# Kernel tuning notes

Hardware: AMD Instinct MI355X
Metric: run time of the kernel (lower is better)

The kernel has to match this reference:

```python
import math
import jax, jax.numpy as jnp
import numpy as np

TOP_K, NC, ALPHA, BETA, EPS = 10, 80, 0.5, 6.0, 1e-9
IMG, STRIDES = 640, (8, 16, 32)


def _ciou(box1, box2, eps=1e-7):
    # box1: gt [bs,n,1,4], box2: pred [bs,1,na,4] -> [bs,n,na,1]
    b1x1, b1y1, b1x2, b1y2 = jnp.split(box1, 4, axis=-1)
    b2x1, b2y1, b2x2, b2y2 = jnp.split(box2, 4, axis=-1)
    w1, h1 = b1x2 - b1x1, b1y2 - b1y1 + eps
    w2, h2 = b2x2 - b2x1, b2y2 - b2y1 + eps
    inter = jnp.clip(jnp.minimum(b1x2, b2x2) - jnp.maximum(b1x1, b2x1), 0.0) * \
            jnp.clip(jnp.minimum(b1y2, b2y2) - jnp.maximum(b1y1, b2y1), 0.0)
    union = w1 * h1 + w2 * h2 - inter + eps
    iou = inter / union
    cw = jnp.maximum(b1x2, b2x2) - jnp.minimum(b1x1, b2x1)
    ch = jnp.maximum(b1y2, b2y2) - jnp.minimum(b1y1, b2y1)
    c2 = cw ** 2 + ch ** 2 + eps
    rho2 = ((b2x1 + b2x2 - b1x1 - b1x2) ** 2 + (b2y1 + b2y2 - b1y1 - b1y2) ** 2) / 4.0
    v = (4.0 / math.pi ** 2) * (jnp.arctan(w2 / h2) - jnp.arctan(w1 / h1)) ** 2
    alpha = jax.lax.stop_gradient(v / (v - iou + (1.0 + eps)))
    return iou - (rho2 / c2 + v * alpha)


def _assign(score, p_box, anchors, gt_labels, gt_box, mask):
    bs, na, nc = score.shape
    n = gt_box.shape[1]
    labels = gt_labels[..., 0].astype(jnp.int32)      # [bs,n]
    valid = mask > 0                                  # [bs,n,1] valid-gt mask
    # --- candidate mask: anchor center strictly inside gt box ---
    lt, rb = gt_box[..., :2], gt_box[..., 2:]
    d = jnp.concatenate([anchors[None, None] - lt[:, :, None],
                         rb[:, :, None] - anchors[None, None]], -1)  # [bs,n,na,4]
    mask_in_gts = d.min(-1) > 1e-9                    # [bs,n,na]
    mask_gts = mask_in_gts & valid
    # --- per-(gt,anchor) class score and CIoU overlap ---
    gathered = score[jnp.arange(bs)[:, None], :, labels]          # [bs,n,na]
    bbox_scores = jnp.where(mask_gts, gathered, 0.0)
    ov = _ciou(gt_box[:, :, None], p_box[:, None])[..., 0]        # [bs,n,na]
    overlaps = jnp.where(mask_gts, jnp.clip(ov, 0.0), 0.0)
    metric = jnp.where(mask_gts,
                       jnp.where(mask_gts, gathered, 1.0) ** ALPHA * overlaps ** BETA,
                       0.0)
    # --- top-k candidates per gt; suppress duplicated indices ---
    _, top_id = jax.lax.top_k(metric, TOP_K)          # [bs,n,TOP_K]
    top_id = jnp.where(valid, top_id, 0)
    bi = jnp.arange(bs)[:, None, None]
    ni = jnp.arange(n)[None, :, None]
    count = jnp.zeros((bs, n, na), jnp.int32).at[bi, ni, top_id].add(1)
    count = jnp.where(count > 1, 0, count)
    mask_pos = count.astype(metric.dtype) * mask_in_gts.astype(metric.dtype) * mask  # [bs,n,na]
    fg = mask_pos.sum(1)                              # [bs,na]
    # --- resolve anchors claimed by multiple gts via max overlap ---
    max_over = (jnp.arange(n)[None, :, None] == jnp.argmax(overlaps, 1)[:, None, :]).astype(metric.dtype)
    mask_pos = jnp.where(fg[:, None, :] > 1, max_over, mask_pos)
    fg = mask_pos.sum(1)
    # --- gather targets ---
    gt_idx = jnp.argmax(mask_pos, 1)                  # [bs,na]
    target_labels = jnp.clip(jnp.take_along_axis(labels, gt_idx, 1), 0)
    target_bboxes = jnp.take_along_axis(gt_box, gt_idx[..., None], 1)  # [bs,na,4]
    ts = jax.nn.one_hot(target_labels, NC, dtype=metric.dtype)
    ts = jnp.where(fg[..., None] > 0, ts, 0.0)
    # --- task-aligned score normalization ---
    metric = metric * mask_pos
    pos_metrics = metric.max(-1, keepdims=True)
    pos_overlaps = (overlaps * mask_pos).max(-1, keepdims=True)
    norm_metric = metric * pos_overlaps / (pos_metrics + EPS)
    target_scores = ts * norm_metric.max(1)[..., None]               # [bs,na,NC]
    return target_bboxes, target_scores, fg > 0


def setup_inputs() -> dict:
    key = jax.random.key(0)
    ks = jax.random.split(key, 8)
    bs, n_max = 16, 64
    # anchor points: grid cell centers for strides 8/16/32 at 640x640
    pts = []
    for s in STRIDES:
        g = IMG // s
        c = (jnp.arange(g, dtype=jnp.float32) + 0.5) * s
        gy, gx = jnp.meshgrid(c, c, indexing='ij')
        pts.append(jnp.stack([gx.ravel(), gy.ravel()], -1))
    anchors = jnp.concatenate(pts, 0)                 # [8400,2]
    na = anchors.shape[0]
    # predicted boxes centered near anchor points
    wh = jax.random.uniform(ks[0], (bs, na, 2), minval=8.0, maxval=128.0)
    ctr = anchors[None] + jax.random.normal(ks[1], (bs, na, 2)) * 4.0
    p_box = jnp.concatenate([ctr - wh / 2, ctr + wh / 2], -1)
    score = jax.random.uniform(ks[2], (bs, na, NC))
    # ground-truth boxes (valid x1<x2, y1<y2)
    gwh = jax.random.uniform(ks[3], (bs, n_max, 2), minval=16.0, maxval=256.0)
    gctr = jax.random.uniform(ks[4], (bs, n_max, 2), minval=0.0, maxval=float(IMG))
    gt_box = jnp.concatenate([gctr - gwh / 2, gctr + gwh / 2], -1)
    gt_labels = jax.random.randint(ks[5], (bs, n_max, 1), 0, NC)
    nvalid = jax.random.randint(ks[6], (bs, 1), 8, n_max + 1)
    mask = (jnp.arange(n_max)[None, :] < nvalid).astype(jnp.float32)[..., None]
    return {"score": score, "p_box": p_box, "anchors": anchors,
            "gt_labels": gt_labels, "gt_box": gt_box, "mask": mask}


def reference(score, p_box, anchors, gt_labels, gt_box, mask):
    return _assign(score, p_box, anchors, gt_labels, gt_box, mask)
```

## Files before the change

kernel.cpp:

```cpp
#include <hip/hip_runtime.h>
#include <math.h>

#define BS   16
#define NMAX 64
#define NA   8400
#define NCLS 80
#define TOPK 10
#define NTH  512
#define KPT  17
#define NWAVE (NTH/64)

typedef unsigned long long u64;

__global__ __launch_bounds__(NTH) void k1_fused(
    const float* __restrict__ score,
    const float* __restrict__ p_box,
    const float* __restrict__ anchors,
    const int*   __restrict__ gt_labels,
    const float* __restrict__ gt_box,
    const float* __restrict__ mask,
    float* __restrict__ overlaps,
    float* __restrict__ metric,
    u64*   __restrict__ mask64)
{
    int row = blockIdx.x;
    if (mask[row] <= 0.f) return;
    int b = row >> 6;
    int n = row & 63;
    const float* gb = gt_box + (size_t)row * 4;
    float gx1 = gb[0], gy1 = gb[1], gx2 = gb[2], gy2 = gb[3];
    int lbl = gt_labels[row];
    float w1 = gx2 - gx1;
    float h1 = gy2 - gy1 + 1e-7f;
    float at1 = atanf(w1 / h1);
    float area1 = w1 * h1;

    float* ovr = overlaps + (size_t)row * NA;
    float* mtr = metric   + (size_t)row * NA;
    const float* sc = score + (size_t)b * NA * NCLS + lbl;
    const float* pb = p_box + (size_t)b * NA * 4;

    int tid = threadIdx.x;
    u64 key[KPT];
#pragma unroll
    for (int k = 0; k < KPT; k++) {
        int a = tid + k * NTH;
        u64 kk = 0ull;
        if (a < NA) {
            float ov = 0.f, mt = 0.f;
            float ax = anchors[a * 2], ay = anchors[a * 2 + 1];
            float dmin = fminf(fminf(ax - gx1, ay - gy1), fminf(gx2 - ax, gy2 - ay));
            if (dmin > 1e-9f) {
                float px1 = pb[a*4], py1 = pb[a*4+1], px2 = pb[a*4+2], py2 = pb[a*4+3];
                float w2 = px2 - px1;
                float h2 = py2 - py1 + 1e-7f;
                float iw = fminf(gx2, px2) - fmaxf(gx1, px1);
                float ih = fminf(gy2, py2) - fmaxf(gy1, py1);
                float inter = fmaxf(iw, 0.f) * fmaxf(ih, 0.f);
                float uni = area1 + w2 * h2 - inter + 1e-7f;
                float iou = inter / uni;
                float cw = fmaxf(gx2, px2) - fminf(gx1, px1);
                float ch = fmaxf(gy2, py2) - fminf(gy1, py1);
                float c2 = cw * cw + ch * ch + 1e-7f;
                float dx = (px1 + px2 - gx1 - gx2);
                float dy = (py1 + py2 - gy1 - gy2);
                float rho2 = (dx * dx + dy * dy) * 0.25f;
                float dat = atanf(w2 / h2) - at1;
                float v = (4.0f / (float)(M_PI * M_PI)) * dat * dat;
                float alpha = v / (v - iou + (1.0f + 1e-7f));
                float ciou = iou - (rho2 / c2 + v * alpha);
                ov = fmaxf(ciou, 0.f);
                float gath = sc[(size_t)a * NCLS];
                float ov2 = ov * ov;
                mt = sqrtf(gath) * ov2 * ov2 * ov2;
            }
            ovr[a] = ov;
            mtr[a] = mt;
            kk = ((u64)__float_as_uint(mt) << 32) | (unsigned)(~a);
        }
        key[k] = kk;
    }

    __shared__ u64 wred[NWAVE];
    __shared__ u64 swin_s;
    __shared__ int sel[TOPK];
    for (int it = 0; it < TOPK; it++) {
        u64 m = 0ull;
#pragma unroll
        for (int k = 0; k < KPT; k++) m = (key[k] > m) ? key[k] : m;
#pragma unroll
        for (int off = 32; off > 0; off >>= 1) {
            u64 o = __shfl_xor(m, off);
            if (o > m) m = o;
        }
        if ((tid & 63) == 0) wred[tid >> 6] = m;
        __syncthreads();
        if (tid == 0) {
            u64 w = wred[0];
#pragma unroll
            for (int j = 1; j < NWAVE; j++) if (wred[j] > w) w = wred[j];
            swin_s = w;
            sel[it] = (int)(~(unsigned)(w & 0xffffffffu));
        }
        __syncthreads();
        u64 win = swin_s;
#pragma unroll
        for (int k = 0; k < KPT; k++) if (key[k] == win) key[k] = 0ull;
    }
    if (tid < TOPK) {
        int a = sel[tid];
        float ax = anchors[a * 2], ay = anchors[a * 2 + 1];
        float dmin = fminf(fminf(ax - gx1, ay - gy1), fminf(gx2 - ax, gy2 - ay));
        if (dmin > 1e-9f)
            atomicOr(&mask64[(size_t)b * NA + a], 1ull << n);
    }
}

__global__ __launch_bounds__(256) void k3_resolve(
    const float* __restrict__ overlaps,
    const float* __restrict__ metric,
    const u64*   __restrict__ mask64,
    const float* __restrict__ mask,
    const float* __restrict__ gt_box,
    int* __restrict__ gt_idx,
    unsigned char* __restrict__ fg_arr,
    float* __restrict__ out_bbox,
    float* __restrict__ out_fg,
    float* __restrict__ pos_metrics,
    float* __restrict__ pos_overlaps)
{
    int i = blockIdx.x * 256 + threadIdx.x;
    if (i >= BS * NA) return;
    int b = i / NA, a = i - b * NA;
    u64 bits = mask64[i];
    int fg0 = __popcll(bits);
    int gi, fg;
    if (fg0 > 1) {
        const float* ov = overlaps + (size_t)b * NMAX * NA + a;
        const float* mrow = mask + b * NMAX;
        float best = -1.f; int argn = 0;
        for (int nn = 0; nn < NMAX; nn++) {
            float v = (mrow[nn] > 0.f) ? ov[(size_t)nn * NA] : 0.f;
            if (v > best) { best = v; argn = nn; }
        }
        gi = argn; fg = 1;
    } else {
        gi = fg0 ? (__ffsll(bits) - 1) : 0;
        fg = fg0;
    }
    gt_idx[i] = gi;
    fg_arr[i] = (unsigned char)fg;
    out_fg[i] = fg ? 1.f : 0.f;
    int r = b * NMAX + gi;
    float4 bb = *(const float4*)(gt_box + (size_t)r * 4);
    ((float4*)out_bbox)[i] = bb;
    if (fg) {
        float m = metric[(size_t)r * NA + a];
        float o = overlaps[(size_t)r * NA + a];
        atomicMax((int*)&pos_metrics[r],  __float_as_int(m));
        atomicMax((int*)&pos_overlaps[r], __float_as_int(o));
    }
}

__global__ __launch_bounds__(256) void k5_sparse(
    const float* __restrict__ metric,
    const int*   __restrict__ gt_idx,
    const unsigned char* __restrict__ fg_arr,
    const int*   __restrict__ gt_labels,
    const float* __restrict__ pos_metrics,
    const float* __restrict__ pos_overlaps,
    float* __restrict__ out_scores)
{
    int i = blockIdx.x * 256 + threadIdx.x;
    if (i >= BS * NA) return;
    if (!fg_arr[i]) return;
    int b = i / NA, a = i - b * NA;
    int r = b * NMAX + gt_idx[i];
    int lbl = gt_labels[r]; if (lbl < 0) lbl = 0;
    float m = metric[(size_t)r * NA + a];
    float val = m * pos_overlaps[r] / (pos_metrics[r] + 1e-9f);
    out_scores[(size_t)i * NCLS + lbl] = val;
}

extern "C" void kernel_launch(void* const* d_in, const int* in_sizes, int n_in,
                              void* d_out, int out_size, void* d_ws, size_t ws_size,
                              hipStream_t stream) {
    (void)in_sizes; (void)n_in; (void)out_size; (void)ws_size;
    const float* score     = (const float*)d_in[0];
    const float* p_box     = (const float*)d_in[1];
    const float* anchors   = (const float*)d_in[2];
    const int*   gt_labels = (const int*)d_in[3];
    const float* gt_box    = (const float*)d_in[4];
    const float* mask      = (const float*)d_in[5];

    const size_t plane = (size_t)BS * NMAX * NA;
    float* overlaps = (float*)d_ws;
    float* metric   = overlaps + plane;
    u64*   mask64   = (u64*)(metric + plane);
    int*   gt_idx   = (int*)(mask64 + (size_t)BS * NA);
    unsigned char* fg_arr = (unsigned char*)(gt_idx + (size_t)BS * NA);
    float* pos_metrics  = (float*)(fg_arr + (((size_t)BS * NA + 7) / 8) * 8);
    float* pos_overlaps = pos_metrics + (size_t)BS * NMAX;

    float* out_bbox   = (float*)d_out;
    float* out_scores = out_bbox + (size_t)BS * NA * 4;
    float* out_fg     = out_scores + (size_t)BS * NA * NCLS;

    hipMemsetAsync(mask64, 0, (size_t)BS * NA * sizeof(u64), stream);
    hipMemsetAsync(pos_metrics, 0, 2 * (size_t)BS * NMAX * sizeof(float), stream);
    hipMemsetAsync(out_scores, 0, (size_t)BS * NA * NCLS * sizeof(float), stream);

    hipLaunchKernelGGL(k1_fused, dim3(BS * NMAX), dim3(NTH), 0, stream,
                       score, p_box, anchors, gt_labels, gt_box, mask,
                       overlaps, metric, mask64);
    hipLaunchKernelGGL(k3_resolve, dim3((BS * NA + 255) / 256), dim3(256), 0, stream,
                       overlaps, metric, mask64, mask, gt_box,
                       gt_idx, fg_arr, out_bbox, out_fg, pos_metrics, pos_overlaps);
    hipLaunchKernelGGL(k5_sparse, dim3((BS * NA + 255) / 256), dim3(256), 0, stream,
                       metric, gt_idx, fg_arr, gt_labels,
                       pos_metrics, pos_overlaps, out_scores);
}
```

Measured before the change: 173.3 us.

## Drop dense overlap/metric planes; split top-k per half and recompute CIoU on conflicts

The fused kernel no longer writes the full [bs,n,na] overlaps and metric planes to workspace. Each gt row is now split across two blocks that each produce a local top-10 with overlaps. A small merge kernel selects the final top-10 and records anchor, metric and overlap per slot. The resolve kernel looks up single-assignment anchors from these slots and recomputes CIoU against all gts only for multi-assigned anchors. This removes a large volume of global writes and reads, at the cost of an extra launch and redundant CIoU/atan work on conflict anchors.

```diff
diff --git a/kernel.cpp b/kernel.cpp
--- a/kernel.cpp
+++ b/kernel.cpp
@@ -6,27 +6,49 @@
 #define NA   8400
 #define NCLS 80
 #define TOPK 10
-#define NTH  512
+#define HALF 4200
+#define NTH  256
 #define KPT  17
-#define NWAVE (NTH/64)
 
 typedef unsigned long long u64;
 
-__global__ __launch_bounds__(NTH) void k1_fused(
+__device__ __forceinline__ float ciou_ov(
+    float gx1, float gy1, float gx2, float gy2, float at1, float area1,
+    float px1, float py1, float px2, float py2)
+{
+    float w2 = px2 - px1;
+    float h2 = py2 - py1 + 1e-7f;
+    float iw = fminf(gx2, px2) - fmaxf(gx1, px1);
+    float ih = fminf(gy2, py2) - fmaxf(gy1, py1);
+    float inter = fmaxf(iw, 0.f) * fmaxf(ih, 0.f);
+    float uni = area1 + w2 * h2 - inter + 1e-7f;
+    float iou = inter / uni;
+    float cw = fmaxf(gx2, px2) - fminf(gx1, px1);
+    float ch = fmaxf(gy2, py2) - fminf(gy1, py1);
+    float c2 = cw * cw + ch * ch + 1e-7f;
+    float dx = (px1 + px2 - gx1 - gx2);
+    float dy = (py1 + py2 - gy1 - gy2);
+    float rho2 = (dx * dx + dy * dy) * 0.25f;
+    float dat = atanf(w2 / h2) - at1;
+    float v = (4.0f / (float)(M_PI * M_PI)) * dat * dat;
+    float alpha = v / (v - iou + (1.0f + 1e-7f));
+    return iou - (rho2 / c2 + v * alpha);
+}
+
+__global__ __launch_bounds__(NTH) void k1a(
     const float* __restrict__ score,
     const float* __restrict__ p_box,
     const float* __restrict__ anchors,
     const int*   __restrict__ gt_labels,
     const float* __restrict__ gt_box,
     const float* __restrict__ mask,
-    float* __restrict__ overlaps,
-    float* __restrict__ metric,
-    u64*   __restrict__ mask64)
-{
-    int row = blockIdx.x;
+    u64*   __restrict__ cand_key,
+    float* __restrict__ cand_ov)
+{
+    int row  = blockIdx.x >> 1;
+    int half = blockIdx.x & 1;
     if (mask[row] <= 0.f) return;
     int b = row >> 6;
-    int n = row & 63;
     const float* gb = gt_box + (size_t)row * 4;
     float gx1 = gb[0], gy1 = gb[1], gx2 = gb[2], gy2 = gb[3];
     int lbl = gt_labels[row];
@@ -35,55 +57,39 @@
     float at1 = atanf(w1 / h1);
     float area1 = w1 * h1;
 
-    float* ovr = overlaps + (size_t)row * NA;
-    float* mtr = metric   + (size_t)row * NA;
     const float* sc = score + (size_t)b * NA * NCLS + lbl;
-    const float* pb = p_box + (size_t)b * NA * 4;
-
+    const float4* pb = (const float4*)(p_box + (size_t)b * NA * 4);
     int tid = threadIdx.x;
-    u64 key[KPT];
+    int abase = half * HALF;
+
+    u64   key[KPT];
+    float ovr[KPT];
 #pragma unroll
     for (int k = 0; k < KPT; k++) {
-        int a = tid + k * NTH;
-        u64 kk = 0ull;
-        if (a < NA) {
-            float ov = 0.f, mt = 0.f;
+        int ai = tid + k * NTH;
+        u64 kk = 0ull; float ov = 0.f;
+        if (ai < HALF) {
+            int a = abase + ai;
             float ax = anchors[a * 2], ay = anchors[a * 2 + 1];
             float dmin = fminf(fminf(ax - gx1, ay - gy1), fminf(gx2 - ax, gy2 - ay));
+            float mt = 0.f;
             if (dmin > 1e-9f) {
-                float px1 = pb[a*4], py1 = pb[a*4+1], px2 = pb[a*4+2], py2 = pb[a*4+3];
-                float w2 = px2 - px1;
-                float h2 = py2 - py1 + 1e-7f;
-                float iw = fminf(gx2, px2) - fmaxf(gx1, px1);
-                float ih = fminf(gy2, py2) - fmaxf(gy1, py1);
-                float inter = fmaxf(iw, 0.f) * fmaxf(ih, 0.f);
-                float uni = area1 + w2 * h2 - inter + 1e-7f;
-                float iou = inter / uni;
-                float cw = fmaxf(gx2, px2) - fminf(gx1, px1);
-                float ch = fmaxf(gy2, py2) - fminf(gy1, py1);
-                float c2 = cw * cw + ch * ch + 1e-7f;
-                float dx = (px1 + px2 - gx1 - gx2);
-                float dy = (py1 + py2 - gy1 - gy2);
-                float rho2 = (dx * dx + dy * dy) * 0.25f;
-                float dat = atanf(w2 / h2) - at1;
-                float v = (4.0f / (float)(M_PI * M_PI)) * dat * dat;
-                float alpha = v / (v - iou + (1.0f + 1e-7f));
-                float ciou = iou - (rho2 / c2 + v * alpha);
-                ov = fmaxf(ciou, 0.f);
+                float4 pv = pb[a];
+                ov = fmaxf(ciou_ov(gx1, gy1, gx2, gy2, at1, area1,
+                                   pv.x, pv.y, pv.z, pv.w), 0.f);
                 float gath = sc[(size_t)a * NCLS];
-                float ov2 = ov * ov;
-                mt = sqrtf(gath) * ov2 * ov2 * ov2;
+                float o2 = ov * ov;
+                mt = sqrtf(gath) * o2 * o2 * o2;
             }
-            ovr[a] = ov;
-            mtr[a] = mt;
             kk = ((u64)__float_as_uint(mt) << 32) | (unsigned)(~a);
         }
-        key[k] = kk;
-    }
-
-    __shared__ u64 wred[NWAVE];
-    __shared__ u64 swin_s;
-    __shared__ int sel[TOPK];
+        key[k] = kk; ovr[k] = ov;
+    }
+
+    __shared__ u64 wred[NTH / 64];
+    __shared__ u64 swin;
+    __shared__ u64 skey[TOPK];
+    __shared__ float sov[TOPK];
     for (int it = 0; it < TOPK; it++) {
         u64 m = 0ull;
 #pragma unroll
@@ -98,87 +104,157 @@
         if (tid == 0) {
             u64 w = wred[0];
 #pragma unroll
-            for (int j = 1; j < NWAVE; j++) if (wred[j] > w) w = wred[j];
-            swin_s = w;
-            sel[it] = (int)(~(unsigned)(w & 0xffffffffu));
+            for (int j = 1; j < NTH / 64; j++) if (wred[j] > w) w = wred[j];
+            swin = w; skey[it] = w;
         }
         __syncthreads();
-        u64 win = swin_s;
-#pragma unroll
-        for (int k = 0; k < KPT; k++) if (key[k] == win) key[k] = 0ull;
-    }
+        u64 win = swin;
+#pragma unroll
+        for (int k = 0; k < KPT; k++)
+            if (key[k] == win) { sov[it] = ovr[k]; key[k] = 0ull; }
+    }
+    __syncthreads();
     if (tid < TOPK) {
-        int a = sel[tid];
+        size_t o = (size_t)row * 20 + half * TOPK + tid;
+        cand_key[o] = skey[tid];
+        cand_ov[o]  = sov[tid];
+    }
+}
+
+__global__ __launch_bounds__(256) void k1b(
+    const float* __restrict__ anchors,
+    const float* __restrict__ gt_box,
+    const float* __restrict__ mask,
+    const u64*   __restrict__ cand_key,
+    const float* __restrict__ cand_ov,
+    u64*   __restrict__ mask64,
+    int*   __restrict__ fin_a,
+    float* __restrict__ fin_mt,
+    float* __restrict__ fin_ov)
+{
+    int row = blockIdx.x * 256 + threadIdx.x;
+    if (row >= BS * NMAX) return;
+    if (mask[row] <= 0.f) return;
+    int b = row >> 6, n = row & 63;
+    u64 k[20];
+#pragma unroll
+    for (int j = 0; j < 20; j++) k[j] = cand_key[(size_t)row * 20 + j];
+    const float* gb = gt_box + (size_t)row * 4;
+    float gx1 = gb[0], gy1 = gb[1], gx2 = gb[2], gy2 = gb[3];
+    for (int it = 0; it < TOPK; it++) {
+        int bj = 0; u64 m = k[0];
+#pragma unroll
+        for (int j = 1; j < 20; j++) if (k[j] > m) { m = k[j]; bj = j; }
+        k[bj] = 0ull;
+        int a = (int)(~(unsigned)(m & 0xffffffffu));
+        float mt = __uint_as_float((unsigned)(m >> 32));
+        float ov = cand_ov[(size_t)row * 20 + bj];
         float ax = anchors[a * 2], ay = anchors[a * 2 + 1];
         float dmin = fminf(fminf(ax - gx1, ay - gy1), fminf(gx2 - ax, gy2 - ay));
-        if (dmin > 1e-9f)
+        int slot = row * TOPK + it;
+        if (dmin > 1e-9f) {
             atomicOr(&mask64[(size_t)b * NA + a], 1ull << n);
+            fin_a[slot] = a; fin_mt[slot] = mt; fin_ov[slot] = ov;
+        } else {
+            fin_a[slot] = -1;
+        }
     }
 }
 
 __global__ __launch_bounds__(256) void k3_resolve(
-    const float* __restrict__ overlaps,
-    const float* __restrict__ metric,
+    const float* __restrict__ score,
+    const float* __restrict__ p_box,
+    const float* __restrict__ anchors,
+    const int*   __restrict__ gt_labels,
+    const float* __restrict__ gt_box,
+    const float* __restrict__ mask,
     const u64*   __restrict__ mask64,
-    const float* __restrict__ mask,
-    const float* __restrict__ gt_box,
+    const int*   __restrict__ fin_a,
+    const float* __restrict__ fin_mt,
+    const float* __restrict__ fin_ov,
     int* __restrict__ gt_idx,
     unsigned char* __restrict__ fg_arr,
+    float* __restrict__ tgt_mt,
     float* __restrict__ out_bbox,
     float* __restrict__ out_fg,
-    float* __restrict__ pos_metrics,
-    float* __restrict__ pos_overlaps)
+    float* __restrict__ pos_mt,
+    float* __restrict__ pos_ov)
 {
     int i = blockIdx.x * 256 + threadIdx.x;
     if (i >= BS * NA) return;
     int b = i / NA, a = i - b * NA;
     u64 bits = mask64[i];
     int fg0 = __popcll(bits);
-    int gi, fg;
-    if (fg0 > 1) {
-        const float* ov = overlaps + (size_t)b * NMAX * NA + a;
+    int gi = 0, fg = 0;
+    float mt = 0.f, ov = 0.f;
+    if (fg0 == 1) {
+        gi = __ffsll(bits) - 1;
+        int r = b * NMAX + gi;
+#pragma unroll
+        for (int s = 0; s < TOPK; s++) {
+            if (fin_a[r * TOPK + s] == a) {
+                mt = fin_mt[r * TOPK + s];
+                ov = fin_ov[r * TOPK + s];
+            }
+        }
+        fg = 1;
+    } else if (fg0 > 1) {
+        float ax = anchors[a * 2], ay = anchors[a * 2 + 1];
+        float4 pv = ((const float4*)(p_box + (size_t)b * NA * 4))[a];
+        const float* gbB = gt_box + (size_t)b * NMAX * 4;
         const float* mrow = mask + b * NMAX;
         float best = -1.f; int argn = 0;
         for (int nn = 0; nn < NMAX; nn++) {
-            float v = (mrow[nn] > 0.f) ? ov[(size_t)nn * NA] : 0.f;
+            float v = 0.f;
+            if (mrow[nn] > 0.f) {
+                float gx1 = gbB[nn*4], gy1 = gbB[nn*4+1], gx2 = gbB[nn*4+2], gy2 = gbB[nn*4+3];
+                float dmin = fminf(fminf(ax - gx1, ay - gy1), fminf(gx2 - ax, gy2 - ay));
+                if (dmin > 1e-9f) {
+                    float w1 = gx2 - gx1;
+                    float h1 = gy2 - gy1 + 1e-7f;
+                    float at1 = atanf(w1 / h1);
+                    v = fmaxf(ciou_ov(gx1, gy1, gx2, gy2, at1, w1 * h1,
+                                      pv.x, pv.y, pv.z, pv.w), 0.f);
+                }
+            }
             if (v > best) { best = v; argn = nn; }
         }
         gi = argn; fg = 1;
-    } else {
-        gi = fg0 ? (__ffsll(bits) - 1) : 0;
-        fg = fg0;
-    }
+        ov = fmaxf(best, 0.f);
+        int lbl = gt_labels[b * NMAX + argn]; if (lbl < 0) lbl = 0;
+        float gath = score[((size_t)b * NA + a) * NCLS + lbl];
+        float o2 = ov * ov;
+        mt = sqrtf(gath) * o2 * o2 * o2;
+    }
+    int r = b * NMAX + gi;
     gt_idx[i] = gi;
     fg_arr[i] = (unsigned char)fg;
+    tgt_mt[i] = mt;
     out_fg[i] = fg ? 1.f : 0.f;
-    int r = b * NMAX + gi;
-    float4 bb = *(const float4*)(gt_box + (size_t)r * 4);
+    float4 bb = ((const float4*)gt_box)[r];
     ((float4*)out_bbox)[i] = bb;
     if (fg) {
-        float m = metric[(size_t)r * NA + a];
-        float o = overlaps[(size_t)r * NA + a];
-        atomicMax((int*)&pos_metrics[r],  __float_as_int(m));
-        atomicMax((int*)&pos_overlaps[r], __float_as_int(o));
+        atomicMax((int*)&pos_mt[r], __float_as_int(mt));
+        atomicMax((int*)&pos_ov[r], __float_as_int(ov));
     }
 }
 
 __global__ __launch_bounds__(256) void k5_sparse(
-    const float* __restrict__ metric,
     const int*   __restrict__ gt_idx,
     const unsigned char* __restrict__ fg_arr,
+    const float* __restrict__ tgt_mt,
     const int*   __restrict__ gt_labels,
-    const float* __restrict__ pos_metrics,
-    const float* __restrict__ pos_overlaps,
+    const float* __restrict__ pos_mt,
+    const float* __restrict__ pos_ov,
     float* __restrict__ out_scores)
 {
     int i = blockIdx.x * 256 + threadIdx.x;
     if (i >= BS * NA) return;
     if (!fg_arr[i]) return;
-    int b = i / NA, a = i - b * NA;
+    int b = i / NA;
     int r = b * NMAX + gt_idx[i];
     int lbl = gt_labels[r]; if (lbl < 0) lbl = 0;
-    float m = metric[(size_t)r * NA + a];
-    float val = m * pos_overlaps[r] / (pos_metrics[r] + 1e-9f);
+    float val = tgt_mt[i] * pos_ov[r] / (pos_mt[r] + 1e-9f);
     out_scores[(size_t)i * NCLS + lbl] = val;
 }
 
@@ -193,30 +269,38 @@
     const float* gt_box    = (const float*)d_in[4];
     const float* mask      = (const float*)d_in[5];
 
-    const size_t plane = (size_t)BS * NMAX * NA;
-    float* overlaps = (float*)d_ws;
-    float* metric   = overlaps + plane;
-    u64*   mask64   = (u64*)(metric + plane);
-    int*   gt_idx   = (int*)(mask64 + (size_t)BS * NA);
-    unsigned char* fg_arr = (unsigned char*)(gt_idx + (size_t)BS * NA);
-    float* pos_metrics  = (float*)(fg_arr + (((size_t)BS * NA + 7) / 8) * 8);
-    float* pos_overlaps = pos_metrics + (size_t)BS * NMAX;
+    const int ROWS = BS * NMAX;
+    char* w = (char*)d_ws;
+    u64*   cand_key = (u64*)w;                  w += (size_t)ROWS * 20 * 8;
+    float* cand_ov  = (float*)w;                w += (size_t)ROWS * 20 * 4;
+    u64*   mask64   = (u64*)w;                  w += (size_t)BS * NA * 8;
+    int*   fin_a    = (int*)w;                  w += (size_t)ROWS * TOPK * 4;
+    float* fin_mt   = (float*)w;                w += (size_t)ROWS * TOPK * 4;
+    float* fin_ov   = (float*)w;                w += (size_t)ROWS * TOPK * 4;
+    int*   gt_idx   = (int*)w;                  w += (size_t)BS * NA * 4;
+    float* tgt_mt   = (float*)w;                w += (size_t)BS * NA * 4;
+    float* pos_mt   = (float*)w;                w += (size_t)ROWS * 4;
+    float* pos_ov   = (float*)w;                w += (size_t)ROWS * 4;
+    unsigned char* fg_arr = (unsigned char*)w;  w += (size_t)BS * NA;
 
     float* out_bbox   = (float*)d_out;
     float* out_scores = out_bbox + (size_t)BS * NA * 4;
     float* out_fg     = out_scores + (size_t)BS * NA * NCLS;
 
-    hipMemsetAsync(mask64, 0, (size_t)BS * NA * sizeof(u64), stream);
-    hipMemsetAsync(pos_metrics, 0, 2 * (size_t)BS * NMAX * sizeof(float), stream);
-    hipMemsetAsync(out_scores, 0, (size_t)BS * NA * NCLS * sizeof(float), stream);
-
-    hipLaunchKernelGGL(k1_fused, dim3(BS * NMAX), dim3(NTH), 0, stream,
+    hipMemsetAsync(mask64, 0, (size_t)BS * NA * 8, stream);
+    hipMemsetAsync(pos_mt, 0, (size_t)ROWS * 4 * 2, stream);
+    hipMemsetAsync(out_scores, 0, (size_t)BS * NA * NCLS * 4, stream);
+
+    hipLaunchKernelGGL(k1a, dim3(ROWS * 2), dim3(NTH), 0, stream,
                        score, p_box, anchors, gt_labels, gt_box, mask,
-                       overlaps, metric, mask64);
+                       cand_key, cand_ov);
+    hipLaunchKernelGGL(k1b, dim3((ROWS + 255) / 256), dim3(256), 0, stream,
+                       anchors, gt_box, mask, cand_key, cand_ov,
+                       mask64, fin_a, fin_mt, fin_ov);
     hipLaunchKernelGGL(k3_resolve, dim3((BS * NA + 255) / 256), dim3(256), 0, stream,
-                       overlaps, metric, mask64, mask, gt_box,
-                       gt_idx, fg_arr, out_bbox, out_fg, pos_metrics, pos_overlaps);
+                       score, p_box, anchors, gt_labels, gt_box, mask,
+                       mask64, fin_a, fin_mt, fin_ov,
+                       gt_idx, fg_arr, tgt_mt, out_bbox, out_fg, pos_mt, pos_ov);
     hipLaunchKernelGGL(k5_sparse, dim3((BS * NA + 255) / 256), dim3(256), 0, stream,
-                       metric, gt_idx, fg_arr, gt_labels,
-                       pos_metrics, pos_overlaps, out_scores);
-}
+                       gt_idx, fg_arr, tgt_mt, gt_labels, pos_mt, pos_ov, out_scores);
+}
```

Measured after the change: 185.3 us. 1.07x slower.
